# Optimization experiments

Measured on AMD Instinct MI355X. Metric: run time of the kernel, lower is better.

The kernel has to match this reference:

```python
import jax, jax.numpy as jnp
import numpy as np

N = 16777216  # flattened neuron count


def setup_inputs() -> dict:
    key = jax.random.key(0)
    k1, k2, k3 = jax.random.split(key, 3)
    x = jax.random.normal(k1, (1, N), dtype=jnp.float32)
    lower = jax.random.normal(k2, (1, N), dtype=jnp.float32)
    # guarantee lower <= upper (module asserts lower_out <= upper_out)
    upper = lower + jnp.abs(jax.random.normal(k3, (1, N), dtype=jnp.float32))
    return {"x": x, "lower": lower, "upper": upper}


def reference(x, lower, upper):
    # self.layer is the ReLU being abstracted
    x_out = jnp.maximum(x, 0.0)

    neg = upper <= 0.0          # branch 1: fully inactive -> bounds stay 0
    pos = lower >= 0.0          # branch 2: fully active (checked after neg)
    crossing = (~neg) & (~pos)  # branch 3: unstable neuron

    # safe slope: u / (u - l); denom > 0 whenever crossing is true
    denom = jnp.where(crossing, upper - lower, 1.0)
    slope = upper / denom

    # faithful to the torch code: active case sets BOTH bounds to u;
    # crossing case: lower_out = alpha * l (alpha = 1), upper_out = slope * u
    lower_out = jnp.where(neg, 0.0, jnp.where(pos, upper, lower))
    upper_out = jnp.where(neg, 0.0, jnp.where(pos, upper, slope * upper))

    return x_out, lower_out, upper_out
```

## Files before the change

kernel.cpp:

```cpp
#include <hip/hip_runtime.h>


#define UNROLL 4

typedef float f32x4 __attribute__((ext_vector_type(4)));

__device__ __forceinline__ void deeppoly_relu_one(float xf, float lf, float uf,
                                                  float& xo, float& lo_o, float& up_o) {
    xo = fmaxf(xf, 0.0f);
    const bool neg = (uf <= 0.0f);
    const bool pos = (lf >= 0.0f);
    const bool crossing = (!neg) && (!pos);
    const float denom = crossing ? (uf - lf) : 1.0f;
    const float su = (uf / denom) * uf;
    lo_o = neg ? 0.0f : (pos ? uf : lf);
    up_o = neg ? 0.0f : (pos ? uf : su);
}

__device__ __forceinline__ void relu_vec4(f32x4 xv, f32x4 lv, f32x4 uv,
                                          f32x4& xo, f32x4& lo_o, f32x4& up_o) {
    #pragma unroll
    for (int j = 0; j < 4; ++j) {
        float a, b, c;
        deeppoly_relu_one(xv[j], lv[j], uv[j], a, b, c);
        xo[j] = a; lo_o[j] = b; up_o[j] = c;
    }
}

__global__ void __launch_bounds__(256) deeppoly_relu_kernel(
    const f32x4* __restrict__ x,
    const f32x4* __restrict__ lo,
    const f32x4* __restrict__ up,
    f32x4* __restrict__ x_out,
    f32x4* __restrict__ lo_out,
    f32x4* __restrict__ up_out,
    int n4)
{
    const int stride = gridDim.x * blockDim.x;
    int base = blockIdx.x * blockDim.x + threadIdx.x;

    for (; base + (UNROLL - 1) * stride < n4; base += UNROLL * stride) {
        f32x4 xv[UNROLL], lv[UNROLL], uv[UNROLL];
        #pragma unroll
        for (int k = 0; k < UNROLL; ++k) {
            const int i = base + k * stride;
            xv[k] = __builtin_nontemporal_load(&x[i]);
            lv[k] = __builtin_nontemporal_load(&lo[i]);
            uv[k] = __builtin_nontemporal_load(&up[i]);
        }
        #pragma unroll
        for (int k = 0; k < UNROLL; ++k) {
            f32x4 xo, lv_o, uv_o;
            relu_vec4(xv[k], lv[k], uv[k], xo, lv_o, uv_o);
            const int i = base + k * stride;
            __builtin_nontemporal_store(xo,   &x_out[i]);
            __builtin_nontemporal_store(lv_o, &lo_out[i]);
            __builtin_nontemporal_store(uv_o, &up_out[i]);
        }
    }
    for (; base < n4; base += stride) {
        f32x4 xv = __builtin_nontemporal_load(&x[base]);
        f32x4 lv = __builtin_nontemporal_load(&lo[base]);
        f32x4 uv = __builtin_nontemporal_load(&up[base]);
        f32x4 xo, lv_o, uv_o;
        relu_vec4(xv, lv, uv, xo, lv_o, uv_o);
        __builtin_nontemporal_store(xo,   &x_out[base]);
        __builtin_nontemporal_store(lv_o, &lo_out[base]);
        __builtin_nontemporal_store(uv_o, &up_out[base]);
    }
}

__global__ void deeppoly_relu_tail(
    const float* __restrict__ x,
    const float* __restrict__ lo,
    const float* __restrict__ up,
    float* __restrict__ x_out,
    float* __restrict__ lo_out,
    float* __restrict__ up_out,
    int start, int n)
{
    int i = start + blockIdx.x * blockDim.x + threadIdx.x;
    if (i < n) {
        float xo, lo_o, up_o;
        deeppoly_relu_one(x[i], lo[i], up[i], xo, lo_o, up_o);
        x_out[i] = xo; lo_out[i] = lo_o; up_out[i] = up_o;
    }
}

extern "C" void kernel_launch(void* const* d_in, const int* in_sizes, int n_in,
                              void* d_out, int out_size, void* d_ws, size_t ws_size,
                              hipStream_t stream) {
    const float* x  = (const float*)d_in[0];
    const float* lo = (const float*)d_in[1];
    const float* up = (const float*)d_in[2];
    float* out = (float*)d_out;

    const int n = in_sizes[0];
    float* x_out  = out;
    float* lo_out = out + (size_t)n;
    float* up_out = out + 2 * (size_t)n;

    const int n4 = n / 4;
    const int block = 256;
    int grid = (n4 + block * UNROLL - 1) / (block * UNROLL);
    if (grid > 8192) grid = 8192;
    if (grid > 0) {
        deeppoly_relu_kernel<<<grid, block, 0, stream>>>(
            (const f32x4*)x, (const f32x4*)lo, (const f32x4*)up,
            (f32x4*)x_out, (f32x4*)lo_out, (f32x4*)up_out, n4);
    }

    const int tail_start = n4 * 4;
    const int tail = n - tail_start;
    if (tail > 0) {
        deeppoly_relu_tail<<<(tail + 255) / 256, 256, 0, stream>>>(
            x, lo, up, x_out, lo_out, up_out, tail_start, n);
    }
}
```

Measured before the change: 82.08 us.

## Split fused ReLU kernel into separate x and bounds kernels with block-tiled unroll

```diff
diff --git a/kernel.cpp b/kernel.cpp
--- a/kernel.cpp
+++ b/kernel.cpp
@@ -1,13 +1,19 @@
 #include <hip/hip_runtime.h>
 
 
-#define UNROLL 4
+#define U 8
 
 typedef float f32x4 __attribute__((ext_vector_type(4)));
 
-__device__ __forceinline__ void deeppoly_relu_one(float xf, float lf, float uf,
-                                                  float& xo, float& lo_o, float& up_o) {
-    xo = fmaxf(xf, 0.0f);
+__device__ __forceinline__ f32x4 nt_load(const f32x4* p) {
+    return __builtin_nontemporal_load(p);
+}
+__device__ __forceinline__ void nt_store(f32x4* p, f32x4 v) {
+    __builtin_nontemporal_store(v, p);
+}
+
+__device__ __forceinline__ void bounds_one(float lf, float uf,
+                                           float& lo_o, float& up_o) {
     const bool neg = (uf <= 0.0f);
     const bool pos = (lf >= 0.0f);
     const bool crossing = (!neg) && (!pos);
@@ -17,73 +23,90 @@
     up_o = neg ? 0.0f : (pos ? uf : su);
 }
 
-__device__ __forceinline__ void relu_vec4(f32x4 xv, f32x4 lv, f32x4 uv,
-                                          f32x4& xo, f32x4& lo_o, f32x4& up_o) {
-    #pragma unroll
-    for (int j = 0; j < 4; ++j) {
-        float a, b, c;
-        deeppoly_relu_one(xv[j], lv[j], uv[j], a, b, c);
-        xo[j] = a; lo_o[j] = b; up_o[j] = c;
+__global__ void __launch_bounds__(256) relu_x_kernel(
+    const f32x4* __restrict__ x, f32x4* __restrict__ x_out, int n4)
+{
+    const int tile = blockDim.x * U;
+    const int ntiles = n4 / tile;
+    for (int t = blockIdx.x; t < ntiles; t += gridDim.x) {
+        const long long base = (long long)t * tile + threadIdx.x;
+        f32x4 v[U];
+        #pragma unroll
+        for (int k = 0; k < U; ++k) v[k] = nt_load(&x[base + k * blockDim.x]);
+        #pragma unroll
+        for (int k = 0; k < U; ++k) {
+            f32x4 r;
+            r.x = fmaxf(v[k].x, 0.0f); r.y = fmaxf(v[k].y, 0.0f);
+            r.z = fmaxf(v[k].z, 0.0f); r.w = fmaxf(v[k].w, 0.0f);
+            nt_store(&x_out[base + k * blockDim.x], r);
+        }
+    }
+    const int rem = ntiles * tile;
+    for (int i = rem + blockIdx.x * blockDim.x + threadIdx.x; i < n4;
+         i += gridDim.x * blockDim.x) {
+        f32x4 v = nt_load(&x[i]);
+        f32x4 r;
+        r.x = fmaxf(v.x, 0.0f); r.y = fmaxf(v.y, 0.0f);
+        r.z = fmaxf(v.z, 0.0f); r.w = fmaxf(v.w, 0.0f);
+        nt_store(&x_out[i], r);
     }
 }
 
-__global__ void __launch_bounds__(256) deeppoly_relu_kernel(
-    const f32x4* __restrict__ x,
-    const f32x4* __restrict__ lo,
-    const f32x4* __restrict__ up,
-    f32x4* __restrict__ x_out,
-    f32x4* __restrict__ lo_out,
-    f32x4* __restrict__ up_out,
-    int n4)
+__global__ void __launch_bounds__(256) relu_bounds_kernel(
+    const f32x4* __restrict__ lo, const f32x4* __restrict__ up,
+    f32x4* __restrict__ lo_out, f32x4* __restrict__ up_out, int n4)
 {
-    const int stride = gridDim.x * blockDim.x;
-    int base = blockIdx.x * blockDim.x + threadIdx.x;
-
-    for (; base + (UNROLL - 1) * stride < n4; base += UNROLL * stride) {
-        f32x4 xv[UNROLL], lv[UNROLL], uv[UNROLL];
+    const int tile = blockDim.x * U;
+    const int ntiles = n4 / tile;
+    for (int t = blockIdx.x; t < ntiles; t += gridDim.x) {
+        const long long base = (long long)t * tile + threadIdx.x;
+        f32x4 lv[U], uv[U];
         #pragma unroll
-        for (int k = 0; k < UNROLL; ++k) {
-            const int i = base + k * stride;
-            xv[k] = __builtin_nontemporal_load(&x[i]);
-            lv[k] = __builtin_nontemporal_load(&lo[i]);
-            uv[k] = __builtin_nontemporal_load(&up[i]);
+        for (int k = 0; k < U; ++k) {
+            lv[k] = nt_load(&lo[base + k * blockDim.x]);
+            uv[k] = nt_load(&up[base + k * blockDim.x]);
         }
         #pragma unroll
-        for (int k = 0; k < UNROLL; ++k) {
-            f32x4 xo, lv_o, uv_o;
-            relu_vec4(xv[k], lv[k], uv[k], xo, lv_o, uv_o);
-            const int i = base + k * stride;
-            __builtin_nontemporal_store(xo,   &x_out[i]);
-            __builtin_nontemporal_store(lv_o, &lo_out[i]);
-            __builtin_nontemporal_store(uv_o, &up_out[i]);
+        for (int k = 0; k < U; ++k) {
+            f32x4 lo_o, up_o;
+            #pragma unroll
+            for (int j = 0; j < 4; ++j) {
+                float a, b;
+                bounds_one(lv[k][j], uv[k][j], a, b);
+                lo_o[j] = a; up_o[j] = b;
+            }
+            nt_store(&lo_out[base + k * blockDim.x], lo_o);
+            nt_store(&up_out[base + k * blockDim.x], up_o);
         }
     }
-    for (; base < n4; base += stride) {
-        f32x4 xv = __builtin_nontemporal_load(&x[base]);
-        f32x4 lv = __builtin_nontemporal_load(&lo[base]);
-        f32x4 uv = __builtin_nontemporal_load(&up[base]);
-        f32x4 xo, lv_o, uv_o;
-        relu_vec4(xv, lv, uv, xo, lv_o, uv_o);
-        __builtin_nontemporal_store(xo,   &x_out[base]);
-        __builtin_nontemporal_store(lv_o, &lo_out[base]);
-        __builtin_nontemporal_store(uv_o, &up_out[base]);
+    const int rem = ntiles * tile;
+    for (int i = rem + blockIdx.x * blockDim.x + threadIdx.x; i < n4;
+         i += gridDim.x * blockDim.x) {
+        f32x4 lv = nt_load(&lo[i]);
+        f32x4 uv = nt_load(&up[i]);
+        f32x4 lo_o, up_o;
+        #pragma unroll
+        for (int j = 0; j < 4; ++j) {
+            float a, b;
+            bounds_one(lv[j], uv[j], a, b);
+            lo_o[j] = a; up_o[j] = b;
+        }
+        nt_store(&lo_out[i], lo_o);
+        nt_store(&up_out[i], up_o);
     }
 }
 
 __global__ void deeppoly_relu_tail(
-    const float* __restrict__ x,
-    const float* __restrict__ lo,
-    const float* __restrict__ up,
-    float* __restrict__ x_out,
-    float* __restrict__ lo_out,
-    float* __restrict__ up_out,
-    int start, int n)
+    const float* __restrict__ x, const float* __restrict__ lo,
+    const float* __restrict__ up, float* __restrict__ x_out,
+    float* __restrict__ lo_out, float* __restrict__ up_out, int start, int n)
 {
     int i = start + blockIdx.x * blockDim.x + threadIdx.x;
     if (i < n) {
-        float xo, lo_o, up_o;
-        deeppoly_relu_one(x[i], lo[i], up[i], xo, lo_o, up_o);
-        x_out[i] = xo; lo_out[i] = lo_o; up_out[i] = up_o;
+        x_out[i] = fmaxf(x[i], 0.0f);
+        float a, b;
+        bounds_one(lo[i], up[i], a, b);
+        lo_out[i] = a; up_out[i] = b;
     }
 }
 
@@ -102,13 +125,16 @@
 
     const int n4 = n / 4;
     const int block = 256;
-    int grid = (n4 + block * UNROLL - 1) / (block * UNROLL);
-    if (grid > 8192) grid = 8192;
-    if (grid > 0) {
-        deeppoly_relu_kernel<<<grid, block, 0, stream>>>(
-            (const f32x4*)x, (const f32x4*)lo, (const f32x4*)up,
-            (f32x4*)x_out, (f32x4*)lo_out, (f32x4*)up_out, n4);
-    }
+    const int tile = block * U;
+    const int ntiles = n4 / tile;
+
+    int gridA = ntiles > 0 ? (ntiles < 2048 ? ntiles : 2048) : 1;
+    int gridB = ntiles > 0 ? (ntiles < 2048 ? ntiles : 2048) : 1;
+
+    relu_x_kernel<<<gridA, block, 0, stream>>>(
+        (const f32x4*)x, (f32x4*)x_out, n4);
+    relu_bounds_kernel<<<gridB, block, 0, stream>>>(
+        (const f32x4*)lo, (const f32x4*)up, (f32x4*)lo_out, (f32x4*)up_out, n4);
 
     const int tail_start = n4 * 4;
     const int tail = n - tail_start;
```

Result: faster. 71.03 us (-13.5%).
